# Performance work log

Measured on AMD Instinct MI355X. Metric: run time of the kernel, lower is better.

## Reference

```python
import jax, jax.numpy as jnp
import numpy as np

G = 512        # molecules per batch
N = 24         # atoms per molecule
D = G * N      # total padded nodes = 12288
DIM = 64       # fingerprint embedding dim
VOCAB = 4096   # fingerprint vocabulary
HL = 3         # hidden_layer (message-passing rounds)
OL = 2         # output_layer


def setup_inputs() -> dict:
    key = jax.random.key(0)
    ks = jax.random.split(key, 8)
    # Block-diagonal padded adjacency (pad(..., 0) in the original): symmetric 0/1
    # blocks on the diagonal, zeros elsewhere.
    rng = np.random.default_rng(0)
    A = np.zeros((D, D), dtype=np.float32)
    for g in range(G):
        blk = (rng.random((N, N)) < 0.3).astype(np.float32)
        blk = np.maximum(blk, blk.T)
        np.fill_diagonal(blk, 0.0)
        s = g * N
        A[s:s + N, s:s + N] = blk
    scale = DIM ** -0.5
    return {
        "fingerprints": jax.random.randint(ks[0], (D,), 0, VOCAB),
        "segment_ids": jnp.repeat(jnp.arange(G), N),  # graph id per node
        "A": jnp.asarray(A),
        "emb_table": jax.random.normal(ks[1], (VOCAB, DIM), jnp.float32) * 0.1,
        "W_fp": jax.random.normal(ks[2], (HL, DIM, DIM), jnp.float32) * scale,
        "b_fp": jnp.zeros((HL, DIM), jnp.float32),
        "W_out": jax.random.normal(ks[3], (OL, DIM, DIM), jnp.float32) * scale,
        "b_out": jnp.zeros((OL, DIM), jnp.float32),
        "W_prop": jax.random.normal(ks[4], (2, DIM), jnp.float32) * scale,
        "b_prop": jnp.zeros((2,), jnp.float32),
    }


def reference(fingerprints, segment_ids, A, emb_table, W_fp, b_fp,
              W_out, b_out, W_prop, b_prop):
    # embed_fingerprint(fingerprints) -> [D, DIM]
    x = emb_table[fingerprints]
    # hidden_layer rounds: x = x + A @ relu(Linear_i(x))   (update == 'sum')
    for i in range(HL):
        h = jax.nn.relu(x @ W_fp[i].T + b_fp[i])
        x = x + A @ h  # block-diagonal padded dense matmul (the hot op)
    # output == 'sum': per-graph segment sum (sum_axis via torch.split)
    mol = jax.ops.segment_sum(x, segment_ids, num_segments=G)  # [G, DIM]
    y = mol
    for j in range(OL):
        y = jax.nn.relu(y @ W_out[j].T + b_out[j])
    predicted_properties = y @ W_prop.T + b_prop  # [G, 2]
    return predicted_properties
```

## Files before the change

kernel.cpp:

```cpp
#include <hip/hip_runtime.h>

#define G 512
#define N 24
#define DD 12288
#define DIM 64

typedef __fp16 f16x2 __attribute__((ext_vector_type(2)));
typedef __fp16 f16x4 __attribute__((ext_vector_type(4)));
typedef __fp16 f16x8 __attribute__((ext_vector_type(8)));
typedef float  f32x4 __attribute__((ext_vector_type(4)));

#define XSTR 72
#define HSTR 36

union PkU { f16x8 v; f16x4 q[2]; f16x2 h2[4]; };

static __device__ __forceinline__ f16x8 pack8(float4 a, float4 b) {
    PkU u;
    u.h2[0] = __builtin_amdgcn_cvt_pkrtz(a.x, a.y);
    u.h2[1] = __builtin_amdgcn_cvt_pkrtz(a.z, a.w);
    u.h2[2] = __builtin_amdgcn_cvt_pkrtz(b.x, b.y);
    u.h2[3] = __builtin_amdgcn_cvt_pkrtz(b.z, b.w);
    return u.v;
}

__global__ __launch_bounds__(64, 2)
void gnn_wave_kernel(const int* __restrict__ fp,
                     const float* __restrict__ A,
                     const float* __restrict__ emb,
                     const float* __restrict__ W_fp,
                     const float* __restrict__ b_fp,
                     const float* __restrict__ W_out,
                     const float* __restrict__ b_out,
                     const float* __restrict__ W_prop,
                     const float* __restrict__ b_prop,
                     float* __restrict__ out)
{
    const int l  = threadIdx.x;
    const int p  = l & 15;
    const int q4 = l >> 4;
    const int gq = blockIdx.x;
    const long srow = (long)gq * N;

    __shared__ __align__(16) __fp16 Xl[32 * XSTR];
    __shared__ __align__(16) __fp16 Hl[64 * HSTR];
    __shared__ float molv[DIM];
    __shared__ float ybuf[DIM];

    f16x8 wf[3][4][2];
    float bias[3][4];
    #pragma unroll
    for (int lyr = 0; lyr < 3; ++lyr) {
        #pragma unroll
        for (int nt = 0; nt < 4; ++nt) {
            bias[lyr][nt] = b_fp[lyr * DIM + 16 * nt + p];
            #pragma unroll
            for (int s = 0; s < 2; ++s) {
                const float* src = W_fp + lyr * DIM * DIM + (16 * nt + p) * DIM + 32 * s + 8 * q4;
                wf[lyr][nt][s] = pack8(*(const float4*)src, *(const float4*)(src + 4));
            }
        }
    }

    f16x8 a24[2];
    #pragma unroll
    for (int mt = 0; mt < 2; ++mt) {
        int r = 16 * mt + p;
        if (r < N && q4 < 3) {
            const float* src = A + (srow + r) * (long)DD + srow + 8 * q4;
            a24[mt] = pack8(*(const float4*)src, *(const float4*)(src + 4));
        } else {
            f16x8 z = { (__fp16)0, (__fp16)0, (__fp16)0, (__fp16)0,
                        (__fp16)0, (__fp16)0, (__fp16)0, (__fp16)0 };
            a24[mt] = z;
        }
    }

    #pragma unroll
    for (int a = 0; a < N; ++a) {
        int f = fp[gq * N + a];
        float v = emb[(long)f * DIM + l];
        Xl[a * XSTR + l] = (__fp16)v;
    }
    #pragma unroll
    for (int r = N; r < 32; ++r) Xl[r * XSTR + l] = (__fp16)0;

    f32x4 xacc[2][4];
    #pragma unroll
    for (int mt = 0; mt < 2; ++mt)
        #pragma unroll
        for (int nt = 0; nt < 4; ++nt)
            #pragma unroll
            for (int reg = 0; reg < 4; ++reg)
                xacc[mt][nt][reg] =
                    (float)Xl[(16 * mt + 4 * q4 + reg) * XSTR + 16 * nt + p];

    #pragma unroll
    for (int lyr = 0; lyr < 3; ++lyr) {
        f32x4 acc[2][4];
        #pragma unroll
        for (int mt = 0; mt < 2; ++mt)
            #pragma unroll
            for (int nt = 0; nt < 4; ++nt) {
                float b = bias[lyr][nt];
                acc[mt][nt] = (f32x4){ b, b, b, b };
            }
        #pragma unroll
        for (int s = 0; s < 2; ++s) {
            f16x8 xa0 = *(const f16x8*)(&Xl[(p) * XSTR + 32 * s + 8 * q4]);
            f16x8 xa1 = *(const f16x8*)(&Xl[(16 + p) * XSTR + 32 * s + 8 * q4]);
            #pragma unroll
            for (int nt = 0; nt < 4; ++nt) {
                acc[0][nt] = __builtin_amdgcn_mfma_f32_16x16x32_f16(xa0, wf[lyr][nt][s], acc[0][nt], 0, 0, 0);
                acc[1][nt] = __builtin_amdgcn_mfma_f32_16x16x32_f16(xa1, wf[lyr][nt][s], acc[1][nt], 0, 0, 0);
            }
        }

        #pragma unroll
        for (int mt = 0; mt < 2; ++mt)
            #pragma unroll
            for (int nt = 0; nt < 4; ++nt) {
                float h0 = fmaxf(acc[mt][nt][0], 0.f);
                float h1 = fmaxf(acc[mt][nt][1], 0.f);
                float h2 = fmaxf(acc[mt][nt][2], 0.f);
                float h3 = fmaxf(acc[mt][nt][3], 0.f);
                PkU u;
                u.h2[0] = __builtin_amdgcn_cvt_pkrtz(h0, h1);
                u.h2[1] = __builtin_amdgcn_cvt_pkrtz(h2, h3);
                *(f16x4*)(&Hl[(16 * nt + p) * HSTR + 16 * mt + 4 * q4]) = u.q[0];
            }

        #pragma unroll
        for (int nt = 0; nt < 4; ++nt) {
            PkU hb;
            hb.q[0] = *(const f16x4*)(&Hl[(16 * nt + p) * HSTR + 8 * q4]);
            hb.q[1] = *(const f16x4*)(&Hl[(16 * nt + p) * HSTR + 8 * q4 + 4]);
            #pragma unroll
            for (int mt = 0; mt < 2; ++mt)
                xacc[mt][nt] = __builtin_amdgcn_mfma_f32_16x16x32_f16(a24[mt], hb.v, xacc[mt][nt], 0, 0, 0);
        }

        if (lyr < 2) {
            #pragma unroll
            for (int mt = 0; mt < 2; ++mt)
                #pragma unroll
                for (int nt = 0; nt < 4; ++nt)
                    #pragma unroll
                    for (int reg = 0; reg < 4; ++reg)
                        Xl[(16 * mt + 4 * q4 + reg) * XSTR + 16 * nt + p] =
                            (__fp16)xacc[mt][nt][reg];
        }
    }

    #pragma unroll
    for (int nt = 0; nt < 4; ++nt) {
        float part = xacc[0][nt][0] + xacc[0][nt][1] + xacc[0][nt][2] + xacc[0][nt][3];
        float part1 = xacc[1][nt][0] + xacc[1][nt][1] + xacc[1][nt][2] + xacc[1][nt][3];
        part += (q4 < 2) ? part1 : 0.f;
        part += __shfl_xor(part, 16, 64);
        part += __shfl_xor(part, 32, 64);
        if (l < 16) molv[16 * nt + l] = part;
    }

    float accy = b_out[l];
    {
        const float* Wr = W_out + l * DIM;
        #pragma unroll
        for (int k4 = 0; k4 < 16; ++k4) {
            float4 wv = *(const float4*)(Wr + 4 * k4);
            float4 mv = *(const float4*)(&molv[4 * k4]);
            accy += wv.x * mv.x + wv.y * mv.y + wv.z * mv.z + wv.w * mv.w;
        }
    }
    ybuf[l] = fmaxf(accy, 0.f);

    float accz = b_out[DIM + l];
    {
        const float* Wr = W_out + DIM * DIM + l * DIM;
        #pragma unroll
        for (int k4 = 0; k4 < 16; ++k4) {
            float4 wv = *(const float4*)(Wr + 4 * k4);
            float4 yv = *(const float4*)(&ybuf[4 * k4]);
            accz += wv.x * yv.x + wv.y * yv.y + wv.z * yv.z + wv.w * yv.w;
        }
    }
    float z = fmaxf(accz, 0.f);

    float t0 = z * W_prop[l];
    float t1 = z * W_prop[DIM + l];
    #pragma unroll
    for (int off = 1; off < 64; off <<= 1) {
        t0 += __shfl_xor(t0, off, 64);
        t1 += __shfl_xor(t1, off, 64);
    }
    if (l == 0) {
        out[gq * 2 + 0] = t0 + b_prop[0];
        out[gq * 2 + 1] = t1 + b_prop[1];
    }
}

extern "C" void kernel_launch(void* const* d_in, const int* in_sizes, int n_in,
                              void* d_out, int out_size, void* d_ws, size_t ws_size,
                              hipStream_t stream) {
    const int*   fp     = (const int*)  d_in[0];
    const float* A      = (const float*)d_in[2];
    const float* emb    = (const float*)d_in[3];
    const float* W_fp   = (const float*)d_in[4];
    const float* b_fp   = (const float*)d_in[5];
    const float* W_out  = (const float*)d_in[6];
    const float* b_out  = (const float*)d_in[7];
    const float* W_prop = (const float*)d_in[8];
    const float* b_prop = (const float*)d_in[9];
    float* out = (float*)d_out;

    gnn_wave_kernel<<<G, 64, 0, stream>>>(fp, A, emb, W_fp, b_fp,
                                          W_out, b_out, W_prop, b_prop, out);
}
```

Before: 14.09 us.

## Split each molecule's feature columns across four waves per block

```diff
diff --git a/kernel.cpp b/kernel.cpp
--- a/kernel.cpp
+++ b/kernel.cpp
@@ -11,7 +11,7 @@
 typedef float  f32x4 __attribute__((ext_vector_type(4)));
 
 #define XSTR 72
-#define HSTR 36
+#define HSTR 40
 
 union PkU { f16x8 v; f16x4 q[2]; f16x2 h2[4]; };
 
@@ -24,43 +24,39 @@
     return u.v;
 }
 
-__global__ __launch_bounds__(64, 2)
-void gnn_wave_kernel(const int* __restrict__ fp,
-                     const float* __restrict__ A,
-                     const float* __restrict__ emb,
-                     const float* __restrict__ W_fp,
-                     const float* __restrict__ b_fp,
-                     const float* __restrict__ W_out,
-                     const float* __restrict__ b_out,
-                     const float* __restrict__ W_prop,
-                     const float* __restrict__ b_prop,
-                     float* __restrict__ out)
+__global__ __launch_bounds__(256, 2)
+void gnn_kernel(const int* __restrict__ fp,
+                const float* __restrict__ A,
+                const float* __restrict__ emb,
+                const float* __restrict__ W_fp,
+                const float* __restrict__ b_fp,
+                const float* __restrict__ W_out,
+                const float* __restrict__ b_out,
+                const float* __restrict__ W_prop,
+                const float* __restrict__ b_prop,
+                float* __restrict__ out)
 {
-    const int l  = threadIdx.x;
+    const int t  = threadIdx.x;
+    const int l  = t & 63;
+    const int wv = t >> 6;
     const int p  = l & 15;
     const int q4 = l >> 4;
     const int gq = blockIdx.x;
     const long srow = (long)gq * N;
 
-    __shared__ __align__(16) __fp16 Xl[32 * XSTR];
-    __shared__ __align__(16) __fp16 Hl[64 * HSTR];
+    __shared__ __align__(16) __fp16 Xl[2][32][XSTR];
+    __shared__ __align__(16) __fp16 Hl[4][16][HSTR];
     __shared__ float molv[DIM];
     __shared__ float ybuf[DIM];
 
-    f16x8 wf[3][4][2];
-    float bias[3][4];
     #pragma unroll
-    for (int lyr = 0; lyr < 3; ++lyr) {
-        #pragma unroll
-        for (int nt = 0; nt < 4; ++nt) {
-            bias[lyr][nt] = b_fp[lyr * DIM + 16 * nt + p];
-            #pragma unroll
-            for (int s = 0; s < 2; ++s) {
-                const float* src = W_fp + lyr * DIM * DIM + (16 * nt + p) * DIM + 32 * s + 8 * q4;
-                wf[lyr][nt][s] = pack8(*(const float4*)src, *(const float4*)(src + 4));
-            }
-        }
+    for (int i = 0; i < 6; ++i) {
+        int a = 6 * wv + i;
+        int f = fp[gq * N + a];
+        Xl[0][a][l] = (__fp16)emb[(long)f * DIM + l];
     }
+    Xl[0][24 + 2 * wv][l] = (__fp16)0.f;
+    Xl[0][25 + 2 * wv][l] = (__fp16)0.f;
 
     f16x8 a24[2];
     #pragma unroll
@@ -76,126 +72,105 @@
         }
     }
 
+    f16x8 wf[3][2];
+    float bias[3];
     #pragma unroll
-    for (int a = 0; a < N; ++a) {
-        int f = fp[gq * N + a];
-        float v = emb[(long)f * DIM + l];
-        Xl[a * XSTR + l] = (__fp16)v;
+    for (int lyr = 0; lyr < 3; ++lyr) {
+        #pragma unroll
+        for (int s = 0; s < 2; ++s) {
+            const float* src = W_fp + lyr * DIM * DIM + (16 * wv + p) * DIM + 32 * s + 8 * q4;
+            wf[lyr][s] = pack8(*(const float4*)src, *(const float4*)(src + 4));
+        }
+        bias[lyr] = b_fp[lyr * DIM + 16 * wv + p];
     }
-    #pragma unroll
-    for (int r = N; r < 32; ++r) Xl[r * XSTR + l] = (__fp16)0;
 
-    f32x4 xacc[2][4];
+    __syncthreads();
+
+    f32x4 xacc[2];
     #pragma unroll
     for (int mt = 0; mt < 2; ++mt)
         #pragma unroll
-        for (int nt = 0; nt < 4; ++nt)
-            #pragma unroll
-            for (int reg = 0; reg < 4; ++reg)
-                xacc[mt][nt][reg] =
-                    (float)Xl[(16 * mt + 4 * q4 + reg) * XSTR + 16 * nt + p];
+        for (int reg = 0; reg < 4; ++reg)
+            xacc[mt][reg] = (float)Xl[0][16 * mt + 4 * q4 + reg][16 * wv + p];
 
     #pragma unroll
     for (int lyr = 0; lyr < 3; ++lyr) {
-        f32x4 acc[2][4];
-        #pragma unroll
-        for (int mt = 0; mt < 2; ++mt)
-            #pragma unroll
-            for (int nt = 0; nt < 4; ++nt) {
-                float b = bias[lyr][nt];
-                acc[mt][nt] = (f32x4){ b, b, b, b };
-            }
+        const int cur = lyr & 1;
+
+        f32x4 acc0 = { bias[lyr], bias[lyr], bias[lyr], bias[lyr] };
+        f32x4 acc1 = acc0;
         #pragma unroll
         for (int s = 0; s < 2; ++s) {
-            f16x8 xa0 = *(const f16x8*)(&Xl[(p) * XSTR + 32 * s + 8 * q4]);
-            f16x8 xa1 = *(const f16x8*)(&Xl[(16 + p) * XSTR + 32 * s + 8 * q4]);
-            #pragma unroll
-            for (int nt = 0; nt < 4; ++nt) {
-                acc[0][nt] = __builtin_amdgcn_mfma_f32_16x16x32_f16(xa0, wf[lyr][nt][s], acc[0][nt], 0, 0, 0);
-                acc[1][nt] = __builtin_amdgcn_mfma_f32_16x16x32_f16(xa1, wf[lyr][nt][s], acc[1][nt], 0, 0, 0);
-            }
+            f16x8 xa0 = *(const f16x8*)(&Xl[cur][p][32 * s + 8 * q4]);
+            f16x8 xa1 = *(const f16x8*)(&Xl[cur][16 + p][32 * s + 8 * q4]);
+            acc0 = __builtin_amdgcn_mfma_f32_16x16x32_f16(xa0, wf[lyr][s], acc0, 0, 0, 0);
+            acc1 = __builtin_amdgcn_mfma_f32_16x16x32_f16(xa1, wf[lyr][s], acc1, 0, 0, 0);
         }
 
-        #pragma unroll
-        for (int mt = 0; mt < 2; ++mt)
-            #pragma unroll
-            for (int nt = 0; nt < 4; ++nt) {
-                float h0 = fmaxf(acc[mt][nt][0], 0.f);
-                float h1 = fmaxf(acc[mt][nt][1], 0.f);
-                float h2 = fmaxf(acc[mt][nt][2], 0.f);
-                float h3 = fmaxf(acc[mt][nt][3], 0.f);
-                PkU u;
-                u.h2[0] = __builtin_amdgcn_cvt_pkrtz(h0, h1);
-                u.h2[1] = __builtin_amdgcn_cvt_pkrtz(h2, h3);
-                *(f16x4*)(&Hl[(16 * nt + p) * HSTR + 16 * mt + 4 * q4]) = u.q[0];
-            }
-
-        #pragma unroll
-        for (int nt = 0; nt < 4; ++nt) {
-            PkU hb;
-            hb.q[0] = *(const f16x4*)(&Hl[(16 * nt + p) * HSTR + 8 * q4]);
-            hb.q[1] = *(const f16x4*)(&Hl[(16 * nt + p) * HSTR + 8 * q4 + 4]);
-            #pragma unroll
-            for (int mt = 0; mt < 2; ++mt)
-                xacc[mt][nt] = __builtin_amdgcn_mfma_f32_16x16x32_f16(a24[mt], hb.v, xacc[mt][nt], 0, 0, 0);
+        {
+            PkU u0, u1;
+            u0.h2[0] = __builtin_amdgcn_cvt_pkrtz(fmaxf(acc0[0], 0.f), fmaxf(acc0[1], 0.f));
+            u0.h2[1] = __builtin_amdgcn_cvt_pkrtz(fmaxf(acc0[2], 0.f), fmaxf(acc0[3], 0.f));
+            u1.h2[0] = __builtin_amdgcn_cvt_pkrtz(fmaxf(acc1[0], 0.f), fmaxf(acc1[1], 0.f));
+            u1.h2[1] = __builtin_amdgcn_cvt_pkrtz(fmaxf(acc1[2], 0.f), fmaxf(acc1[3], 0.f));
+            *(f16x4*)(&Hl[wv][p][4 * q4])      = u0.q[0];
+            *(f16x4*)(&Hl[wv][p][16 + 4 * q4]) = u1.q[0];
         }
 
+        f16x8 hb = *(const f16x8*)(&Hl[wv][p][8 * q4]);
+        xacc[0] = __builtin_amdgcn_mfma_f32_16x16x32_f16(a24[0], hb, xacc[0], 0, 0, 0);
+        xacc[1] = __builtin_amdgcn_mfma_f32_16x16x32_f16(a24[1], hb, xacc[1], 0, 0, 0);
+
         if (lyr < 2) {
+            const int nxt = cur ^ 1;
             #pragma unroll
             for (int mt = 0; mt < 2; ++mt)
                 #pragma unroll
-                for (int nt = 0; nt < 4; ++nt)
-                    #pragma unroll
-                    for (int reg = 0; reg < 4; ++reg)
-                        Xl[(16 * mt + 4 * q4 + reg) * XSTR + 16 * nt + p] =
-                            (__fp16)xacc[mt][nt][reg];
+                for (int reg = 0; reg < 4; ++reg)
+                    Xl[nxt][16 * mt + 4 * q4 + reg][16 * wv + p] = (__fp16)xacc[mt][reg];
+            __syncthreads();
         }
     }
 
-    #pragma unroll
-    for (int nt = 0; nt < 4; ++nt) {
-        float part = xacc[0][nt][0] + xacc[0][nt][1] + xacc[0][nt][2] + xacc[0][nt][3];
-        float part1 = xacc[1][nt][0] + xacc[1][nt][1] + xacc[1][nt][2] + xacc[1][nt][3];
-        part += (q4 < 2) ? part1 : 0.f;
-        part += __shfl_xor(part, 16, 64);
-        part += __shfl_xor(part, 32, 64);
-        if (l < 16) molv[16 * nt + l] = part;
-    }
+    float part = (xacc[0][0] + xacc[0][1]) + (xacc[0][2] + xacc[0][3])
+               + (xacc[1][0] + xacc[1][1]) + (xacc[1][2] + xacc[1][3]);
+    part += __shfl_xor(part, 16, 64);
+    part += __shfl_xor(part, 32, 64);
+    if (l < 16) molv[16 * wv + l] = part;
+    __syncthreads();
 
-    float accy = b_out[l];
-    {
-        const float* Wr = W_out + l * DIM;
+    if (t < DIM) {
+        float accy = b_out[t];
+        const float* Wr0 = W_out + t * DIM;
         #pragma unroll
         for (int k4 = 0; k4 < 16; ++k4) {
-            float4 wv = *(const float4*)(Wr + 4 * k4);
+            float4 wr = *(const float4*)(Wr0 + 4 * k4);
             float4 mv = *(const float4*)(&molv[4 * k4]);
-            accy += wv.x * mv.x + wv.y * mv.y + wv.z * mv.z + wv.w * mv.w;
+            accy += wr.x * mv.x + wr.y * mv.y + wr.z * mv.z + wr.w * mv.w;
         }
-    }
-    ybuf[l] = fmaxf(accy, 0.f);
+        ybuf[t] = fmaxf(accy, 0.f);
 
-    float accz = b_out[DIM + l];
-    {
-        const float* Wr = W_out + DIM * DIM + l * DIM;
+        float accz = b_out[DIM + t];
+        const float* Wr1 = W_out + DIM * DIM + t * DIM;
         #pragma unroll
         for (int k4 = 0; k4 < 16; ++k4) {
-            float4 wv = *(const float4*)(Wr + 4 * k4);
+            float4 wr = *(const float4*)(Wr1 + 4 * k4);
             float4 yv = *(const float4*)(&ybuf[4 * k4]);
-            accz += wv.x * yv.x + wv.y * yv.y + wv.z * yv.z + wv.w * yv.w;
+            accz += wr.x * yv.x + wr.y * yv.y + wr.z * yv.z + wr.w * yv.w;
         }
-    }
-    float z = fmaxf(accz, 0.f);
+        float z = fmaxf(accz, 0.f);
 
-    float t0 = z * W_prop[l];
-    float t1 = z * W_prop[DIM + l];
-    #pragma unroll
-    for (int off = 1; off < 64; off <<= 1) {
-        t0 += __shfl_xor(t0, off, 64);
-        t1 += __shfl_xor(t1, off, 64);
-    }
-    if (l == 0) {
-        out[gq * 2 + 0] = t0 + b_prop[0];
-        out[gq * 2 + 1] = t1 + b_prop[1];
+        float t0 = z * W_prop[t];
+        float t1 = z * W_prop[DIM + t];
+        #pragma unroll
+        for (int off = 1; off < 64; off <<= 1) {
+            t0 += __shfl_xor(t0, off, 64);
+            t1 += __shfl_xor(t1, off, 64);
+        }
+        if (t == 0) {
+            out[gq * 2 + 0] = t0 + b_prop[0];
+            out[gq * 2 + 1] = t1 + b_prop[1];
+        }
     }
 }
 
@@ -211,8 +186,8 @@
     const float* b_out  = (const float*)d_in[7];
     const float* W_prop = (const float*)d_in[8];
     const float* b_prop = (const float*)d_in[9];
-    float* out = (float*)d_out;
+    float* outp = (float*)d_out;
 
-    gnn_wave_kernel<<<G, 64, 0, stream>>>(fp, A, emb, W_fp, b_fp,
-                                          W_out, b_out, W_prop, b_prop, out);
+    gnn_kernel<<<G, 256, 0, stream>>>(fp, A, emb, W_fp, b_fp,
+                                      W_out, b_out, W_prop, b_prop, outp);
 }
```

Result: faster. 12.38 us (median of 2 runs) (-12.2%).
